# Performance work log

Measured on AMD Instinct MI355X. Metric: run time of the kernel, lower is better.

Reference implementation:

```python
import jax, jax.numpy as jnp
import numpy as np
from jax import lax


def grouped_linear(x, w):
    # x: [d0, d1, G*ws], w: [G, ws, out_per_group] -> [d0, d1, G*out_per_group]
    d0, d1, _ = x.shape
    G, ws, o = w.shape
    x = x.reshape(d0, d1, G, ws)
    return jnp.einsum('btgi,gio->btgh'.replace('h', 'o'), x, w).reshape(d0, d1, G * o)


def gru_layer(x, w_ih, w_hh, b_ih, b_hh):
    # x: [T, H_in]; w_ih/w_hh: [3, H, H_in]; b_ih/b_hh: [3, H]; gate order (r, z, n)
    ih = jnp.einsum('ti,ghi->tgh', x, w_ih) + b_ih  # input projections for all t at once

    def step(h, ih_t):
        hh = jnp.einsum('i,ghi->gh', h, w_hh) + b_hh
        r = jax.nn.sigmoid(ih_t[0] + hh[0])
        z = jax.nn.sigmoid(ih_t[1] + hh[1])
        n = jnp.tanh(ih_t[2] + r * hh[2])
        h_new = n + z * (h - n)
        return h_new, h_new

    h0 = jnp.zeros((w_hh.shape[1],), x.dtype)
    _, ys = lax.scan(step, h0, ih)
    return ys  # [T, H]


def setup_inputs() -> dict:
    key = jax.random.key(0)
    T, B, H = 8192, 1, 512
    HID, G, L = 512, 8, 2
    C_IN, C_OUT, F, KT = 64, 10, 96, 2
    ks = jax.random.split(key, 17)
    s = jnp.float32(0.05)
    return {
        'emb_tbh': jax.random.normal(ks[0], (T, B, H), jnp.float32),
        'c0': jax.random.normal(ks[1], (B, C_IN, T, F), jnp.float32),
        'lin_in_w': jax.random.normal(ks[2], (G, H // G, HID // G), jnp.float32) * s,
        'gru_w_ih': jax.random.normal(ks[3], (L, 3, HID, HID), jnp.float32) * s,
        'gru_w_hh': jax.random.normal(ks[4], (L, 3, HID, HID), jnp.float32) * s,
        'gru_b_ih': jax.random.normal(ks[5], (L, 3, HID), jnp.float32) * s,
        'gru_b_hh': jax.random.normal(ks[6], (L, 3, HID), jnp.float32) * s,
        'gru_skip_w': jax.random.normal(ks[7], (HID, HID), jnp.float32) * s,
        'gru_skip_b': jax.random.normal(ks[8], (HID,), jnp.float32) * s,
        'lin_out_w': jax.random.normal(ks[9], (G, HID // G, HID // G), jnp.float32) * s,
        'df_skip_w': jax.random.normal(ks[10], (HID, H), jnp.float32) * s,
        'df_skip_b': jax.random.normal(ks[11], (HID,), jnp.float32) * s,
        'fc_a_w': jax.random.normal(ks[12], (1, HID), jnp.float32) * s,
        'fc_a_b': jax.random.normal(ks[13], (1,), jnp.float32) * s,
        'df_out_w': jax.random.normal(ks[14], (G, HID // G, (F * C_OUT) // G), jnp.float32) * s,
        'convp_w': jax.random.normal(ks[15], (C_OUT, C_IN, KT, 1), jnp.float32) * s,
        'convp_b': jax.random.normal(ks[16], (C_OUT,), jnp.float32) * s,
    }


def reference(emb_tbh, c0, lin_in_w, gru_w_ih, gru_w_hh, gru_b_ih, gru_b_hh,
              gru_skip_w, gru_skip_b, lin_out_w, df_skip_w, df_skip_b,
              fc_a_w, fc_a_b, df_out_w, convp_w, convp_b):
    T, B, H = emb_tbh.shape  # B == 1 (manual GRU loop assumes it)
    DF_BINS, DF_OUT_CH = 96, 10

    # --- squeezed GRU: grouped linear_in + ReLU, manual GRU layers, skip, grouped linear_out + ReLU
    x = jax.nn.relu(grouped_linear(emb_tbh, lin_in_w))  # [T, B, HID]
    gru_in = x
    h = x[:, 0, :]  # [T, HID], B == 1
    for l in range(gru_w_ih.shape[0]):
        h = gru_layer(h, gru_w_ih[l], gru_w_hh[l], gru_b_ih[l], gru_b_hh[l])
    x = h[:, None, :]
    x = x + (gru_in @ gru_skip_w.T + gru_skip_b)
    x = jax.nn.relu(grouped_linear(x, lin_out_w))  # [T, B, HID]

    # --- skip from embedding + alpha head
    emb = emb_tbh.reshape(B, T, H)  # B==1: pure relabel of dims
    c = x.reshape(B, T, -1)
    c = c + (emb @ df_skip_w.T + df_skip_b)
    alpha = jax.nn.sigmoid(c @ fc_a_w.T + fc_a_b)  # [B, T, 1]

    # --- df_convp: causal time pad (top=1) + Conv2d kernel (2,1), then permute to [B,T,F,Cout]
    c0p = jnp.pad(c0, ((0, 0), (0, 0), (1, 0), (0, 0)))
    c0c = lax.conv_general_dilated(c0p, convp_w, (1, 1), 'VALID',
                                   dimension_numbers=('NCHW', 'OIHW', 'NCHW'))
    c0c = c0c + convp_b[None, :, None, None]
    c0c = jnp.transpose(c0c, (0, 2, 3, 1))  # [B, T, F, Cout]

    # --- df_out: grouped linear + tanh, reshape to coef grid, add conv pathway
    c = jnp.tanh(grouped_linear(c, df_out_w))  # [B, T, F*Cout]
    c = c.reshape(B, T, DF_BINS, DF_OUT_CH) + c0c
    return (c, alpha)
```

## Files before the change

kernel.cpp:

```cpp
#include <hip/hip_runtime.h>
#include <hip/hip_bf16.h>
#include <cstdint>

#define T_STEPS 8192
#define NWG 64

typedef unsigned long long ull;

__device__ __forceinline__ float fast_sigmoid(float v) {
  return __fdividef(1.f, 1.f + __expf(-v));
}
__device__ __forceinline__ float fast_tanh(float v) {
  return 1.f - __fdividef(2.f, __expf(2.f * v) + 1.f);
}
__device__ __forceinline__ ull packpair(float v, unsigned tag) {
  return ((ull)__float_as_uint(v) << 32) | (ull)tag;
}
__device__ __forceinline__ float bf_lo(unsigned u) { return __uint_as_float(u << 16); }
__device__ __forceinline__ float bf_hi(unsigned u) { return __uint_as_float(u & 0xFFFF0000u); }

__global__ __launch_bounds__(256) void k_grouped_relu(const float* __restrict__ in,
                                                      const float* __restrict__ W,
                                                      float* __restrict__ out) {
  __shared__ float es[512];
  const int t = blockIdx.x;
  const int tid = threadIdx.x;
  const float* inr = in + (size_t)t * 512;
  ((float2*)es)[tid] = ((const float2*)inr)[tid];
  __syncthreads();
#pragma unroll
  for (int rep = 0; rep < 2; ++rep) {
    int jj = tid + rep * 256;
    int g = jj >> 6, o = jj & 63;
    const float* wp = W + (g << 12) + o;
    const float* ep = es + (g << 6);
    float acc = 0.f;
#pragma unroll 8
    for (int i = 0; i < 64; ++i) acc = fmaf(ep[i], wp[i << 6], acc);
    out[(size_t)t * 512 + jj] = fmaxf(acc, 0.f);
  }
}

__global__ __launch_bounds__(256) void k_gemm_rr(const float* __restrict__ A,
                                                 const float* __restrict__ B,
                                                 const float* __restrict__ bias,
                                                 const float* __restrict__ add,
                                                 float* __restrict__ C, int N) {
  __shared__ float As[64][68];
  __shared__ float Bs[64][68];
  const int bm = blockIdx.x << 6, bn = blockIdx.y << 6;
  const int tid = threadIdx.x;
  const int tx = tid & 15, ty = tid >> 4;
  float acc[4][4] = {};
  for (int k0 = 0; k0 < 512; k0 += 64) {
#pragma unroll
    for (int u = 0; u < 4; ++u) {
      int f4 = (u << 8) + tid;
      int m = f4 >> 4;
      int kq = (f4 & 15) << 2;
      float4 av = *(const float4*)(A + (size_t)(bm + m) * 512 + k0 + kq);
      As[kq + 0][m] = av.x; As[kq + 1][m] = av.y; As[kq + 2][m] = av.z; As[kq + 3][m] = av.w;
      float4 bv = *(const float4*)(B + (size_t)(bn + m) * 512 + k0 + kq);
      Bs[kq + 0][m] = bv.x; Bs[kq + 1][m] = bv.y; Bs[kq + 2][m] = bv.z; Bs[kq + 3][m] = bv.w;
    }
    __syncthreads();
#pragma unroll
    for (int k = 0; k < 64; ++k) {
      float4 a4 = *(const float4*)(&As[k][ty << 2]);
      float4 b4 = *(const float4*)(&Bs[k][tx << 2]);
      float ar[4] = {a4.x, a4.y, a4.z, a4.w};
      float br[4] = {b4.x, b4.y, b4.z, b4.w};
#pragma unroll
      for (int i = 0; i < 4; ++i)
#pragma unroll
        for (int j = 0; j < 4; ++j) acc[i][j] = fmaf(ar[i], br[j], acc[i][j]);
    }
    __syncthreads();
  }
  const int n0 = bn + (tx << 2);
  float4 bsv = *(const float4*)(bias + n0);
#pragma unroll
  for (int i = 0; i < 4; ++i) {
    int m = bm + (ty << 2) + i;
    float4 res;
    res.x = acc[i][0] + bsv.x; res.y = acc[i][1] + bsv.y;
    res.z = acc[i][2] + bsv.z; res.w = acc[i][3] + bsv.w;
    if (add) {
      float4 ad = *(const float4*)(add + (size_t)m * N + n0);
      res.x += ad.x; res.y += ad.y; res.z += ad.z; res.w += ad.w;
    }
    *(float4*)(C + (size_t)m * N + n0) = res;
  }
}

__global__ __launch_bounds__(512, 1) void k_gru_fused(
    const float* __restrict__ ih0,
    const float* __restrict__ Whh0, const float* __restrict__ bhh0,
    const float* __restrict__ Wih1, const float* __restrict__ bih1,
    const float* __restrict__ Whh1, const float* __restrict__ bhh1,
    float* __restrict__ h1seq,
    ull* __restrict__ ring0,
    ull* __restrict__ ring1) {
  __shared__ ushort wl[8][9][512];
  __shared__ float hb[2][1024];
  const int wg = blockIdx.x, tid = threadIdx.x;
  const int w = tid >> 6, l = tid & 63;
  const int base = wg << 3;
  const int r = base + w;

  for (int idx = tid; idx < 8 * 9 * 512; idx += 512) {
    const int k = idx & 511;
    const int rest = idx >> 9;
    const int gi = rest % 9;
    const int rr = rest / 9;
    const int m = gi / 3, g = gi - m * 3;
    const float* srcm = (m == 0) ? Whh0 : ((m == 1) ? Wih1 : Whh1);
    const float v = srcm[((size_t)g << 18) + ((size_t)(base + rr) << 9) + k];
    unsigned u = __float_as_uint(v);
    u += 0x7FFFu + ((u >> 16) & 1u);
    wl[rr][gi][k] = (ushort)(u >> 16);
  }
  float b9[9] = {};
  if (l == 0) {
#pragma unroll
    for (int g = 0; g < 3; ++g) {
      b9[g] = bhh0[(g << 9) + r];
      b9[3 + g] = bih1[(g << 9) + r];
      b9[6 + g] = bhh1[(g << 9) + r];
    }
  }
  __syncthreads();

  float h0own = 0.f, h1own = 0.f;
  const bool isH1 = (w >= 4);
  const int pidx = ((w & 3) << 6) + l;
  const int doff = isH1 ? 512 : 0;

  for (int t = 0; t <= T_STEPS; ++t) {
    float i0 = 0.f, i1 = 0.f, i2 = 0.f;
    if (l == 0 && t < T_STEPS) {
      const float* p = ih0 + (size_t)t * 1536 + r;
      i0 = p[0]; i1 = p[512]; i2 = p[1024];
    }
    {
      ull* sp = isH1 ? (ring1 + ((t & 1) << 9)) : (ring0 + (((t + 1) & 1) << 9));
      const unsigned expm = isH1 ? (unsigned)((t > 0) ? t - 1 : 0) : (unsigned)t;
      ull Pa, Pb;
      for (;;) {
        Pa = __hip_atomic_load(sp + pidx, __ATOMIC_RELAXED, __HIP_MEMORY_SCOPE_AGENT);
        Pb = __hip_atomic_load(sp + pidx + 256, __ATOMIC_RELAXED, __HIP_MEMORY_SCOPE_AGENT);
        bool bad = (((unsigned)Pa) != expm) | (((unsigned)Pb) != expm);
        if (__ballot(bad) == 0ull) break;
      }
      float* dst = hb[t & 1] + doff;
      dst[pidx] = __uint_as_float((unsigned)(Pa >> 32));
      dst[pidx + 256] = __uint_as_float((unsigned)(Pb >> 32));
    }
    __syncthreads();
    const float* hp = hb[t & 1];
    float4 h0a = *(const float4*)(hp + (l << 3));
    float4 h0b = *(const float4*)(hp + (l << 3) + 4);
    float4 h1a = *(const float4*)(hp + 512 + (l << 3));
    float4 h1b = *(const float4*)(hp + 512 + (l << 3) + 4);
    float acc[9];
#pragma unroll
    for (int gi = 0; gi < 9; ++gi) {
      const uint4 wv = *(const uint4*)(&wl[w][gi][l << 3]);
      const float4 ha = (gi < 6) ? h0a : h1a;
      const float4 hc = (gi < 6) ? h0b : h1b;
      float d = bf_lo(wv.x) * ha.x;
      d = fmaf(bf_hi(wv.x), ha.y, d);
      d = fmaf(bf_lo(wv.y), ha.z, d);
      d = fmaf(bf_hi(wv.y), ha.w, d);
      d = fmaf(bf_lo(wv.z), hc.x, d);
      d = fmaf(bf_hi(wv.z), hc.y, d);
      d = fmaf(bf_lo(wv.w), hc.z, d);
      d = fmaf(bf_hi(wv.w), hc.w, d);
      acc[gi] = d;
    }
#pragma unroll
    for (int m = 1; m < 64; m <<= 1)
#pragma unroll
      for (int i = 0; i < 9; ++i) acc[i] += __shfl_xor(acc[i], m);
    if (l == 0) {
      if (t < T_STEPS) {
        float rr = fast_sigmoid(i0 + acc[0] + b9[0]);
        float zz = fast_sigmoid(i1 + acc[1] + b9[1]);
        float nn = fast_tanh(fmaf(rr, acc[2] + b9[2], i2));
        h0own = fmaf(zz, h0own - nn, nn);
        __hip_atomic_store(ring0 + ((t & 1) << 9) + r, packpair(h0own, (unsigned)(t + 1)),
                           __ATOMIC_RELAXED, __HIP_MEMORY_SCOPE_AGENT);
      }
      if (t >= 1) {
        float rr = fast_sigmoid(acc[3] + b9[3] + acc[6] + b9[6]);
        float zz = fast_sigmoid(acc[4] + b9[4] + acc[7] + b9[7]);
        float nn = fast_tanh(fmaf(rr, acc[8] + b9[8], acc[5] + b9[5]));
        h1own = fmaf(zz, h1own - nn, nn);
        __hip_atomic_store(ring1 + (((t + 1) & 1) << 9) + r, packpair(h1own, (unsigned)t),
                           __ATOMIC_RELAXED, __HIP_MEMORY_SCOPE_AGENT);
        h1seq[(size_t)(t - 1) * 512 + r] = h1own;
      }
    }
  }
}

__global__ __launch_bounds__(256) void k_alpha(const float* __restrict__ c,
                                               const float* __restrict__ w,
                                               const float* __restrict__ b,
                                               float* __restrict__ alpha) {
  const int wave = threadIdx.x >> 6, lane = threadIdx.x & 63;
  const int t = (blockIdx.x << 2) + wave;
  const float* cr = c + (size_t)t * 512;
  float acc = 0.f;
#pragma unroll
  for (int q = 0; q < 8; ++q) acc = fmaf(cr[lane + (q << 6)], w[lane + (q << 6)], acc);
#pragma unroll
  for (int m = 32; m; m >>= 1) acc += __shfl_xor(acc, m);
  if (lane == 0) alpha[t] = 1.f / (1.f + __expf(-(acc + b[0])));
}

__global__ __launch_bounds__(256) void k_dfout_conv(const float* __restrict__ c,
                                                    const float* __restrict__ Wd,
                                                    const float* __restrict__ c0,
                                                    const float* __restrict__ wc,
                                                    const float* __restrict__ bc,
                                                    float* __restrict__ out) {
  __shared__ float cs[512];
  __shared__ float A0[64 * 96];
  __shared__ float A1[64 * 96];
  __shared__ float wcs[1280];
  __shared__ float cc[960];
  const int t = blockIdx.x, tid = threadIdx.x;
  ((float2*)cs)[tid] = ((const float2*)(c + (size_t)t * 512))[tid];
  for (int idx = tid; idx < 64 * 96; idx += 256) {
    int ci = idx / 96, f = idx - ci * 96;
    size_t base = (size_t)ci * ((size_t)T_STEPS * 96) + (size_t)t * 96 + f;
    A1[idx] = c0[base];
    A0[idx] = (t == 0) ? 0.f : c0[base - 96];
  }
  for (int idx = tid; idx < 1280; idx += 256) wcs[idx] = wc[idx];
  __syncthreads();
  for (int idx = tid; idx < 960; idx += 256) {
    int f = idx / 10, co = idx - f * 10;
    float acc = bc[co];
    const float* w = wcs + (co << 7);
#pragma unroll 16
    for (int ci = 0; ci < 64; ++ci) {
      acc = fmaf(A0[ci * 96 + f], w[ci * 2 + 0], acc);
      acc = fmaf(A1[ci * 96 + f], w[ci * 2 + 1], acc);
    }
    cc[idx] = acc;
  }
  __syncthreads();
  for (int idx = tid; idx < 960; idx += 256) {
    int g = idx / 120, o = idx - g * 120;
    const float* wp = Wd + g * 7680 + o;
    const float* ep = cs + (g << 6);
    float acc = 0.f;
#pragma unroll 16
    for (int i = 0; i < 64; ++i) acc = fmaf(ep[i], wp[i * 120], acc);
    out[(size_t)t * 960 + idx] = tanhf(acc) + cc[idx];
  }
}

extern "C" void kernel_launch(void* const* d_in, const int* in_sizes, int n_in,
                              void* d_out, int out_size, void* d_ws, size_t ws_size,
                              hipStream_t stream) {
  const float* emb       = (const float*)d_in[0];
  const float* c0        = (const float*)d_in[1];
  const float* lin_in_w  = (const float*)d_in[2];
  const float* w_ih      = (const float*)d_in[3];
  const float* w_hh      = (const float*)d_in[4];
  const float* b_ih      = (const float*)d_in[5];
  const float* b_hh      = (const float*)d_in[6];
  const float* skip_w    = (const float*)d_in[7];
  const float* skip_b    = (const float*)d_in[8];
  const float* lin_out_w = (const float*)d_in[9];
  const float* df_skip_w = (const float*)d_in[10];
  const float* df_skip_b = (const float*)d_in[11];
  const float* fc_a_w    = (const float*)d_in[12];
  const float* fc_a_b    = (const float*)d_in[13];
  const float* df_out_w  = (const float*)d_in[14];
  const float* convp_w   = (const float*)d_in[15];
  const float* convp_b   = (const float*)d_in[16];

  const size_t T = T_STEPS;
  float* x    = (float*)d_ws;
  float* ih   = x + T * 512;
  float* h1   = ih + T * 1536;
  ull* ring0  = (ull*)(h1 + T * 512);
  ull* ring1  = ring0 + 1024;
  float* sbuf = ih;
  float* vbuf = ih + T * 512;
  float* cbuf = ih + 2 * T * 512;
  float* outc = (float*)d_out;
  float* outa = outc + T * 960;

  k_grouped_relu<<<T_STEPS, 256, 0, stream>>>(emb, lin_in_w, x);
  k_gemm_rr<<<dim3(128, 24), 256, 0, stream>>>(x, w_ih, b_ih, nullptr, ih, 1536);
  (void)hipMemsetAsync(ring0, 0, 2048 * sizeof(ull), stream);
  k_gru_fused<<<NWG, 512, 0, stream>>>(ih, w_hh, b_hh,
                                       w_ih + 786432, b_ih + 1536,
                                       w_hh + 786432, b_hh + 1536,
                                       h1, ring0, ring1);
  k_gemm_rr<<<dim3(128, 8), 256, 0, stream>>>(x, skip_w, skip_b, h1, sbuf, 512);
  k_grouped_relu<<<T_STEPS, 256, 0, stream>>>(sbuf, lin_out_w, vbuf);
  k_gemm_rr<<<dim3(128, 8), 256, 0, stream>>>(emb, df_skip_w, df_skip_b, vbuf, cbuf, 512);
  k_alpha<<<T_STEPS / 4, 256, 0, stream>>>(cbuf, fc_a_w, fc_a_b, outa);
  k_dfout_conv<<<T_STEPS, 256, 0, stream>>>(cbuf, df_out_w, c0, convp_w, convp_b, outc);
  (void)in_sizes; (void)n_in; (void)out_size; (void)ws_size;
}
```

Before: 32.44 ms.

## Publish layer-0 hidden state before computing layer-1 gates in fused GRU

Splits the per-step gate computation so the three layer-0 hidden-hidden dot products are reduced and the new layer-0 state is stored to the ring first. The six layer-1 dot products run afterwards, behind a scheduling barrier. This shortens the critical path of the cross-workgroup recurrence, since other workgroups can start polling sooner. The ring polling also changes to read two adjacent entries per thread and write them to LDS as one float2, which gives more contiguous accesses. The cost is two separate shuffle-reduction phases instead of one interleaved batch, which exposes more reduction latency.

```diff
diff --git a/kernel.cpp b/kernel.cpp
--- a/kernel.cpp
+++ b/kernel.cpp
@@ -132,8 +132,8 @@
   __syncthreads();
 
   float h0own = 0.f, h1own = 0.f;
-  const bool isH1 = (w >= 4);
-  const int pidx = ((w & 3) << 6) + l;
+  const bool isH1 = (tid >= 256);
+  const int q = tid & 255;
   const int doff = isH1 ? 512 : 0;
 
   for (int t = 0; t <= T_STEPS; ++t) {
@@ -147,27 +147,61 @@
       const unsigned expm = isH1 ? (unsigned)((t > 0) ? t - 1 : 0) : (unsigned)t;
       ull Pa, Pb;
       for (;;) {
-        Pa = __hip_atomic_load(sp + pidx, __ATOMIC_RELAXED, __HIP_MEMORY_SCOPE_AGENT);
-        Pb = __hip_atomic_load(sp + pidx + 256, __ATOMIC_RELAXED, __HIP_MEMORY_SCOPE_AGENT);
+        Pa = __hip_atomic_load(sp + 2 * q, __ATOMIC_RELAXED, __HIP_MEMORY_SCOPE_AGENT);
+        Pb = __hip_atomic_load(sp + 2 * q + 1, __ATOMIC_RELAXED, __HIP_MEMORY_SCOPE_AGENT);
         bool bad = (((unsigned)Pa) != expm) | (((unsigned)Pb) != expm);
         if (__ballot(bad) == 0ull) break;
       }
-      float* dst = hb[t & 1] + doff;
-      dst[pidx] = __uint_as_float((unsigned)(Pa >> 32));
-      dst[pidx + 256] = __uint_as_float((unsigned)(Pb >> 32));
+      float2 v;
+      v.x = __uint_as_float((unsigned)(Pa >> 32));
+      v.y = __uint_as_float((unsigned)(Pb >> 32));
+      *(float2*)(hb[t & 1] + doff + 2 * q) = v;
     }
     __syncthreads();
     const float* hp = hb[t & 1];
     float4 h0a = *(const float4*)(hp + (l << 3));
     float4 h0b = *(const float4*)(hp + (l << 3) + 4);
+    float a0, a1, a2;
+    {
+      float acc3[3];
+#pragma unroll
+      for (int gi = 0; gi < 3; ++gi) {
+        const uint4 wv = *(const uint4*)(&wl[w][gi][l << 3]);
+        float d = bf_lo(wv.x) * h0a.x;
+        d = fmaf(bf_hi(wv.x), h0a.y, d);
+        d = fmaf(bf_lo(wv.y), h0a.z, d);
+        d = fmaf(bf_hi(wv.y), h0a.w, d);
+        d = fmaf(bf_lo(wv.z), h0b.x, d);
+        d = fmaf(bf_hi(wv.z), h0b.y, d);
+        d = fmaf(bf_lo(wv.w), h0b.z, d);
+        d = fmaf(bf_hi(wv.w), h0b.w, d);
+        acc3[gi] = d;
+      }
+#pragma unroll
+      for (int m = 1; m < 64; m <<= 1) {
+        acc3[0] += __shfl_xor(acc3[0], m);
+        acc3[1] += __shfl_xor(acc3[1], m);
+        acc3[2] += __shfl_xor(acc3[2], m);
+      }
+      a0 = acc3[0]; a1 = acc3[1]; a2 = acc3[2];
+    }
+    if (l == 0 && t < T_STEPS) {
+      float rr = fast_sigmoid(i0 + a0 + b9[0]);
+      float zz = fast_sigmoid(i1 + a1 + b9[1]);
+      float nn = fast_tanh(fmaf(rr, a2 + b9[2], i2));
+      h0own = fmaf(zz, h0own - nn, nn);
+      __hip_atomic_store(ring0 + ((t & 1) << 9) + r, packpair(h0own, (unsigned)(t + 1)),
+                         __ATOMIC_RELAXED, __HIP_MEMORY_SCOPE_AGENT);
+    }
+    __builtin_amdgcn_sched_barrier(0);
     float4 h1a = *(const float4*)(hp + 512 + (l << 3));
     float4 h1b = *(const float4*)(hp + 512 + (l << 3) + 4);
-    float acc[9];
-#pragma unroll
-    for (int gi = 0; gi < 9; ++gi) {
-      const uint4 wv = *(const uint4*)(&wl[w][gi][l << 3]);
-      const float4 ha = (gi < 6) ? h0a : h1a;
-      const float4 hc = (gi < 6) ? h0b : h1b;
+    float acc6[6];
+#pragma unroll
+    for (int gi = 0; gi < 6; ++gi) {
+      const uint4 wv = *(const uint4*)(&wl[w][3 + gi][l << 3]);
+      const float4 ha = (gi < 3) ? h0a : h1a;
+      const float4 hc = (gi < 3) ? h0b : h1b;
       float d = bf_lo(wv.x) * ha.x;
       d = fmaf(bf_hi(wv.x), ha.y, d);
       d = fmaf(bf_lo(wv.y), ha.z, d);
@@ -176,30 +210,20 @@
       d = fmaf(bf_hi(wv.z), hc.y, d);
       d = fmaf(bf_lo(wv.w), hc.z, d);
       d = fmaf(bf_hi(wv.w), hc.w, d);
-      acc[gi] = d;
+      acc6[gi] = d;
     }
 #pragma unroll
     for (int m = 1; m < 64; m <<= 1)
 #pragma unroll
-      for (int i = 0; i < 9; ++i) acc[i] += __shfl_xor(acc[i], m);
-    if (l == 0) {
-      if (t < T_STEPS) {
-        float rr = fast_sigmoid(i0 + acc[0] + b9[0]);
-        float zz = fast_sigmoid(i1 + acc[1] + b9[1]);
-        float nn = fast_tanh(fmaf(rr, acc[2] + b9[2], i2));
-        h0own = fmaf(zz, h0own - nn, nn);
-        __hip_atomic_store(ring0 + ((t & 1) << 9) + r, packpair(h0own, (unsigned)(t + 1)),
-                           __ATOMIC_RELAXED, __HIP_MEMORY_SCOPE_AGENT);
-      }
-      if (t >= 1) {
-        float rr = fast_sigmoid(acc[3] + b9[3] + acc[6] + b9[6]);
-        float zz = fast_sigmoid(acc[4] + b9[4] + acc[7] + b9[7]);
-        float nn = fast_tanh(fmaf(rr, acc[8] + b9[8], acc[5] + b9[5]));
-        h1own = fmaf(zz, h1own - nn, nn);
-        __hip_atomic_store(ring1 + (((t + 1) & 1) << 9) + r, packpair(h1own, (unsigned)t),
-                           __ATOMIC_RELAXED, __HIP_MEMORY_SCOPE_AGENT);
-        h1seq[(size_t)(t - 1) * 512 + r] = h1own;
-      }
+      for (int i = 0; i < 6; ++i) acc6[i] += __shfl_xor(acc6[i], m);
+    if (l == 0 && t >= 1) {
+      float rr = fast_sigmoid(acc6[0] + b9[3] + acc6[3] + b9[6]);
+      float zz = fast_sigmoid(acc6[1] + b9[4] + acc6[4] + b9[7]);
+      float nn = fast_tanh(fmaf(rr, acc6[5] + b9[8], acc6[2] + b9[5]));
+      h1own = fmaf(zz, h1own - nn, nn);
+      __hip_atomic_store(ring1 + (((t + 1) & 1) << 9) + r, packpair(h1own, (unsigned)t),
+                         __ATOMIC_RELAXED, __HIP_MEMORY_SCOPE_AGENT);
+      h1seq[(size_t)(t - 1) * 512 + r] = h1own;
     }
   }
 }
```

Result: no change. 32.17 ms (-0.8%).
